# Performance work log

Hardware: AMD Instinct MI355X
Metric: run time of the kernel (lower is better)

## Reference

```python
import jax, jax.numpy as jnp
import numpy as np

N = 2_000_000
C = 64
B = 16
H = C // 2  # reduction_ratio = 2


def setup_inputs() -> dict:
    key = jax.random.key(0)
    k1, k2, k3, k4, k5, k6 = jax.random.split(key, 6)
    x = jax.random.normal(k1, (N, C), dtype=jnp.float32)
    batch_ids = jnp.sort(jax.random.randint(k2, (N,), 0, B, dtype=jnp.int32))
    # nn.Linear-style params: y = x @ W.T + b
    W1 = jax.random.normal(k3, (H, C), dtype=jnp.float32) * (1.0 / np.sqrt(C))
    b1 = jax.random.normal(k4, (H,), dtype=jnp.float32) * 0.01
    W2 = jax.random.normal(k5, (C, H), dtype=jnp.float32) * (1.0 / np.sqrt(H))
    b2 = jax.random.normal(k6, (C,), dtype=jnp.float32) * 0.01
    return {"x": x, "batch_ids": batch_ids, "W1": W1, "b1": b1, "W2": W2, "b2": b2}


def reference(x, batch_ids, W1, b1, W2, b2):
    # Global avg / max pooling per batch segment -> [B, C]
    sums = jax.ops.segment_sum(x, batch_ids, num_segments=B)
    counts = jax.ops.segment_sum(jnp.ones((x.shape[0],), x.dtype), batch_ids, num_segments=B)
    avg = sums / jnp.maximum(counts, 1.0)[:, None]
    mx = jax.ops.segment_max(x, batch_ids, num_segments=B)

    def mlp(h):  # shared tiny MLP: Linear -> ReLU -> Linear
        return jax.nn.relu(h @ W1.T + b1) @ W2.T + b2

    att = jax.nn.sigmoid(mlp(avg) + mlp(mx))  # [B, C]
    # per-point broadcast multiply-add: x * att[batch] + x
    return x * att[batch_ids] + x
```

## Files before the change

kernel.cpp:

```cpp
#include <hip/hip_runtime.h>
#include <math.h>

#define NCH   64
#define NBAT  16
#define NHID  32
#define NBLK  1024

typedef float    f4 __attribute__((ext_vector_type(4)));
typedef _Float16 h4 __attribute__((ext_vector_type(4)));


__device__ __forceinline__ void atomicMaxF(float* addr, float v) {
    if (v >= 0.0f) atomicMax((int*)addr, __float_as_int(v));
    else           atomicMin((unsigned int*)addr, __float_as_uint(v));
}

__device__ __forceinline__ f4 vmax4(f4 a, f4 b) {
    f4 r;
    r.x = fmaxf(a.x, b.x); r.y = fmaxf(a.y, b.y);
    r.z = fmaxf(a.z, b.z); r.w = fmaxf(a.w, b.w);
    return r;
}

__device__ __forceinline__ int lower_bound_i(const int* __restrict__ a, int n, int v) {
    int lo = 0, hi = n;
    while (lo < hi) {
        const int mid = (lo + hi) >> 1;
        if (a[mid] < v) lo = mid + 1; else hi = mid;
    }
    return lo;
}

__global__ __launch_bounds__(256) void init_kernel(float* ws) {
    const int i = blockIdx.x * blockDim.x + threadIdx.x;
    if (i < 1024) {
        ws[i] = 0.0f;
        ws[1024 + i] = -INFINITY;
    }
}


__global__ __launch_bounds__(256) void pool_stage_kernel(const float* __restrict__ x,
                                                         const int* __restrict__ bid,
                                                         float* __restrict__ wsum,
                                                         float* __restrict__ wmax,
                                                         _Float16* __restrict__ xh,
                                                         int n, int rpb) {
    __shared__ int sstart[NBAT + 1];
    __shared__ f4 ls[256];
    __shared__ f4 lm[256];
    const int t = threadIdx.x;
    if (t <= NBAT) sstart[t] = (t == NBAT) ? n : lower_bound_i(bid, n, t);
    __syncthreads();

    const int c4 = t & 15;
    const int rg = t >> 4;
    const int r0 = blockIdx.x * rpb;
    const int rend = min(r0 + rpb, n);
    const f4 fzero = {0.f, 0.f, 0.f, 0.f};
    const f4 fninf = {-INFINITY, -INFINITY, -INFINITY, -INFINITY};

    for (int b = 0; b < NBAT; ++b) {
        const int lo = max(sstart[b], r0);
        const int hi = min(sstart[b + 1], rend);
        if (lo >= hi) continue;

        f4 s = fzero, m = fninf;
        const int base = lo + rg;
        const int k = (hi > base) ? ((hi - base + 15) >> 4) : 0;
        const float* xp = x + (size_t)base * NCH + c4 * 4;
        _Float16* hp = xh + (size_t)base * NCH + c4 * 4;
        int j = 0;
        for (; j + 4 <= k; j += 4) {
            const f4 v0 = __builtin_nontemporal_load(reinterpret_cast<const f4*>(xp + (size_t)(j + 0) * 16 * NCH));
            const f4 v1 = __builtin_nontemporal_load(reinterpret_cast<const f4*>(xp + (size_t)(j + 1) * 16 * NCH));
            const f4 v2 = __builtin_nontemporal_load(reinterpret_cast<const f4*>(xp + (size_t)(j + 2) * 16 * NCH));
            const f4 v3 = __builtin_nontemporal_load(reinterpret_cast<const f4*>(xp + (size_t)(j + 3) * 16 * NCH));
            s += v0; s += v1; s += v2; s += v3;
            m = vmax4(m, vmax4(vmax4(v0, v1), vmax4(v2, v3)));
            *reinterpret_cast<h4*>(hp + (size_t)(j + 0) * 16 * NCH) = __builtin_convertvector(v0, h4);
            *reinterpret_cast<h4*>(hp + (size_t)(j + 1) * 16 * NCH) = __builtin_convertvector(v1, h4);
            *reinterpret_cast<h4*>(hp + (size_t)(j + 2) * 16 * NCH) = __builtin_convertvector(v2, h4);
            *reinterpret_cast<h4*>(hp + (size_t)(j + 3) * 16 * NCH) = __builtin_convertvector(v3, h4);
        }
        for (; j < k; ++j) {
            const f4 v = __builtin_nontemporal_load(reinterpret_cast<const f4*>(xp + (size_t)j * 16 * NCH));
            s += v; m = vmax4(m, v);
            *reinterpret_cast<h4*>(hp + (size_t)j * 16 * NCH) = __builtin_convertvector(v, h4);
        }

        ls[t] = s; lm[t] = m;
        __syncthreads();
        if (rg == 0) {
            for (int gg = 1; gg < 16; ++gg) {
                s += ls[gg * 16 + c4];
                m = vmax4(m, lm[gg * 16 + c4]);
            }
            float* ps = wsum + b * NCH + c4 * 4;
            atomicAdd(ps + 0, s.x);
            atomicAdd(ps + 1, s.y);
            atomicAdd(ps + 2, s.z);
            atomicAdd(ps + 3, s.w);
            float* pm = wmax + b * NCH + c4 * 4;
            atomicMaxF(pm + 0, m.x);
            atomicMaxF(pm + 1, m.y);
            atomicMaxF(pm + 2, m.z);
            atomicMaxF(pm + 3, m.w);
        }
        __syncthreads();
    }
}

__global__ __launch_bounds__(256) void apply_stage_kernel(const _Float16* __restrict__ xh,
                                                          const int* __restrict__ bid,
                                                          const float* __restrict__ scale,
                                                          float* __restrict__ out,
                                                          int n, int rpb) {
    __shared__ int   sstart[NBAT + 1];
    __shared__ float s_scale[NBAT * NCH];
    const int t = threadIdx.x;
    if (t <= NBAT) sstart[t] = (t == NBAT) ? n : lower_bound_i(bid, n, t);
    for (int i = t; i < NBAT * NCH; i += 256) s_scale[i] = scale[i];
    __syncthreads();

    const int c4 = t & 15;
    const int rg = t >> 4;
    const int r0 = blockIdx.x * rpb;
    const int rend = min(r0 + rpb, n);

    for (int b = 0; b < NBAT; ++b) {
        const int lo = max(sstart[b], r0);
        const int hi = min(sstart[b + 1], rend);
        if (lo >= hi) continue;

        const f4 sc = *reinterpret_cast<const f4*>(s_scale + b * NCH + c4 * 4);
        const int base = lo + rg;
        const int k = (hi > base) ? ((hi - base + 15) >> 4) : 0;
        const _Float16* hp = xh + (size_t)base * NCH + c4 * 4;
        float* op = out + (size_t)base * NCH + c4 * 4;

        int j = 0;
        for (; j + 8 <= k; j += 8) {
            h4 u[8];
#pragma unroll
            for (int q = 0; q < 8; ++q)
                u[q] = *reinterpret_cast<const h4*>(hp + (size_t)(j + q) * 16 * NCH);
#pragma unroll
            for (int q = 0; q < 8; ++q) {
                const f4 v = __builtin_convertvector(u[q], f4) * sc;
                __builtin_nontemporal_store(v, reinterpret_cast<f4*>(op + (size_t)(j + q) * 16 * NCH));
            }
        }
        for (; j < k; ++j) {
            const h4 u = *reinterpret_cast<const h4*>(hp + (size_t)j * 16 * NCH);
            const f4 v = __builtin_convertvector(u, f4) * sc;
            __builtin_nontemporal_store(v, reinterpret_cast<f4*>(op + (size_t)j * 16 * NCH));
        }
    }
}


__global__ __launch_bounds__(256) void pool_kernel(const float* __restrict__ x,
                                                   const int* __restrict__ bid,
                                                   float* __restrict__ wsum,
                                                   float* __restrict__ wmax,
                                                   int n, int rpb) {
    __shared__ int sstart[NBAT + 1];
    __shared__ f4 ls[256];
    __shared__ f4 lm[256];
    const int t = threadIdx.x;
    if (t <= NBAT) sstart[t] = (t == NBAT) ? n : lower_bound_i(bid, n, t);
    __syncthreads();

    const int c4 = t & 15;
    const int rg = t >> 4;
    const int r0 = blockIdx.x * rpb;
    const int rend = min(r0 + rpb, n);
    const f4 fzero = {0.f, 0.f, 0.f, 0.f};
    const f4 fninf = {-INFINITY, -INFINITY, -INFINITY, -INFINITY};

    for (int b = 0; b < NBAT; ++b) {
        const int lo = max(sstart[b], r0);
        const int hi = min(sstart[b + 1], rend);
        if (lo >= hi) continue;

        f4 s = fzero, m = fninf;
        const int base = lo + rg;
        const int k = (hi > base) ? ((hi - base + 15) >> 4) : 0;
        const float* xp = x + (size_t)base * NCH + c4 * 4;
        int j = 0;
        for (; j + 4 <= k; j += 4) {
            const f4 v0 = *reinterpret_cast<const f4*>(xp + (size_t)(j + 0) * 16 * NCH);
            const f4 v1 = *reinterpret_cast<const f4*>(xp + (size_t)(j + 1) * 16 * NCH);
            const f4 v2 = *reinterpret_cast<const f4*>(xp + (size_t)(j + 2) * 16 * NCH);
            const f4 v3 = *reinterpret_cast<const f4*>(xp + (size_t)(j + 3) * 16 * NCH);
            s += v0; s += v1; s += v2; s += v3;
            m = vmax4(m, vmax4(vmax4(v0, v1), vmax4(v2, v3)));
        }
        for (; j < k; ++j) {
            const f4 v = *reinterpret_cast<const f4*>(xp + (size_t)j * 16 * NCH);
            s += v; m = vmax4(m, v);
        }

        ls[t] = s; lm[t] = m;
        __syncthreads();
        if (rg == 0) {
            for (int gg = 1; gg < 16; ++gg) {
                s += ls[gg * 16 + c4];
                m = vmax4(m, lm[gg * 16 + c4]);
            }
            float* ps = wsum + b * NCH + c4 * 4;
            atomicAdd(ps + 0, s.x);
            atomicAdd(ps + 1, s.y);
            atomicAdd(ps + 2, s.z);
            atomicAdd(ps + 3, s.w);
            float* pm = wmax + b * NCH + c4 * 4;
            atomicMaxF(pm + 0, m.x);
            atomicMaxF(pm + 1, m.y);
            atomicMaxF(pm + 2, m.z);
            atomicMaxF(pm + 3, m.w);
        }
        __syncthreads();
    }
}

__global__ __launch_bounds__(256) void apply_kernel(const float* __restrict__ x,
                                                    const int* __restrict__ bid,
                                                    const float* __restrict__ scale,
                                                    float* __restrict__ out,
                                                    int n, int rpb) {
    __shared__ int   sstart[NBAT + 1];
    __shared__ float s_scale[NBAT * NCH];
    const int t = threadIdx.x;
    if (t <= NBAT) sstart[t] = (t == NBAT) ? n : lower_bound_i(bid, n, t);
    for (int i = t; i < NBAT * NCH; i += 256) s_scale[i] = scale[i];
    __syncthreads();

    const int c4 = t & 15;
    const int rg = t >> 4;
    const int r0 = blockIdx.x * rpb;
    const int rend = min(r0 + rpb, n);

    for (int b = NBAT - 1; b >= 0; --b) {
        const int lo = max(sstart[b], r0);
        const int hi = min(sstart[b + 1], rend);
        if (lo >= hi) continue;

        const f4 sc = *reinterpret_cast<const f4*>(s_scale + b * NCH + c4 * 4);
        const int base = lo + rg;
        int k = (hi > base) ? ((hi - base + 15) >> 4) : 0;
        const float* xp = x + (size_t)base * NCH + c4 * 4;
        float* op = out + (size_t)base * NCH + c4 * 4;

        while (k >= 4) {
            k -= 4;
            const f4 v0 = *reinterpret_cast<const f4*>(xp + (size_t)(k + 0) * 16 * NCH);
            const f4 v1 = *reinterpret_cast<const f4*>(xp + (size_t)(k + 1) * 16 * NCH);
            const f4 v2 = *reinterpret_cast<const f4*>(xp + (size_t)(k + 2) * 16 * NCH);
            const f4 v3 = *reinterpret_cast<const f4*>(xp + (size_t)(k + 3) * 16 * NCH);
            __builtin_nontemporal_store(v0 * sc, reinterpret_cast<f4*>(op + (size_t)(k + 0) * 16 * NCH));
            __builtin_nontemporal_store(v1 * sc, reinterpret_cast<f4*>(op + (size_t)(k + 1) * 16 * NCH));
            __builtin_nontemporal_store(v2 * sc, reinterpret_cast<f4*>(op + (size_t)(k + 2) * 16 * NCH));
            __builtin_nontemporal_store(v3 * sc, reinterpret_cast<f4*>(op + (size_t)(k + 3) * 16 * NCH));
        }
        while (k > 0) {
            --k;
            const f4 v = *reinterpret_cast<const f4*>(xp + (size_t)k * 16 * NCH);
            __builtin_nontemporal_store(v * sc, reinterpret_cast<f4*>(op + (size_t)k * 16 * NCH));
        }
    }
}


__global__ __launch_bounds__(512) void mlp_kernel(const float* __restrict__ ws,
                                                  const int* __restrict__ bid,
                                                  const float* __restrict__ W1,
                                                  const float* __restrict__ b1,
                                                  const float* __restrict__ W2,
                                                  const float* __restrict__ b2,
                                                  float* __restrict__ scale_out,
                                                  int n) {
    __shared__ int   sstart[NBAT + 1];
    __shared__ float avg[NBAT * NCH];
    __shared__ float mxs[NBAT * NCH];
    __shared__ float h1a[NBAT * NHID];
    __shared__ float h1m[NBAT * NHID];
    const int t = threadIdx.x;
    if (t <= NBAT) sstart[t] = (t == NBAT) ? n : lower_bound_i(bid, n, t);
    __syncthreads();

    for (int i = t; i < NBAT * NCH; i += 512) {
        const int b = i >> 6;
        const float c = (float)(sstart[b + 1] - sstart[b]);
        avg[i] = ws[i] / fmaxf(c, 1.0f);
        mxs[i] = ws[1024 + i];
    }
    __syncthreads();

    {
        const int b = t >> 5, j = t & 31;
        float sa = b1[j], sm = b1[j];
        const float* w = W1 + j * NCH;
        for (int c = 0; c < NCH; ++c) {
            const float wv = w[c];
            sa += avg[b * NCH + c] * wv;
            sm += mxs[b * NCH + c] * wv;
        }
        h1a[b * NHID + j] = fmaxf(sa, 0.0f);
        h1m[b * NHID + j] = fmaxf(sm, 0.0f);
    }
    __syncthreads();

    for (int i = t; i < NBAT * NCH; i += 512) {
        const int b = i >> 6, c = i & 63;
        float ya = b2[c], ym = b2[c];
        const float* w = W2 + c * NHID;
        for (int j = 0; j < NHID; ++j) {
            const float wv = w[j];
            ya += h1a[b * NHID + j] * wv;
            ym += h1m[b * NHID + j] * wv;
        }
        const float z = ya + ym;
        const float sig = 1.0f / (1.0f + expf(-z));
        scale_out[i] = 1.0f + sig;
    }
}

extern "C" void kernel_launch(void* const* d_in, const int* in_sizes, int n_in,
                              void* d_out, int out_size, void* d_ws, size_t ws_size,
                              hipStream_t stream) {
    const float* x   = (const float*)d_in[0];
    const int*   bid = (const int*)d_in[1];
    const float* W1  = (const float*)d_in[2];
    const float* b1  = (const float*)d_in[3];
    const float* W2  = (const float*)d_in[4];
    const float* b2  = (const float*)d_in[5];
    float* out = (float*)d_out;
    const int n = in_sizes[1];

    float* ws     = (float*)d_ws;
    float* wsum   = ws;
    float* wmax   = ws + 1024;
    float* wscale = ws + 2064;
    _Float16* xh  = (_Float16*)((char*)d_ws + 16384);

    const size_t need = 16384 + (size_t)n * NCH * sizeof(_Float16);
    const bool staged = (ws_size >= need);

    hipLaunchKernelGGL(init_kernel, dim3(4), dim3(256), 0, stream, ws);

    const int rpb = (n + NBLK - 1) / NBLK;
    if (staged) {
        hipLaunchKernelGGL(pool_stage_kernel, dim3(NBLK), dim3(256), 0, stream,
                           x, bid, wsum, wmax, xh, n, rpb);
        hipLaunchKernelGGL(mlp_kernel, dim3(1), dim3(512), 0, stream,
                           ws, bid, W1, b1, W2, b2, wscale, n);
        hipLaunchKernelGGL(apply_stage_kernel, dim3(NBLK), dim3(256), 0, stream,
                           xh, bid, wscale, out, n, rpb);
    } else {
        hipLaunchKernelGGL(pool_kernel, dim3(NBLK), dim3(256), 0, stream,
                           x, bid, wsum, wmax, n, rpb);
        hipLaunchKernelGGL(mlp_kernel, dim3(1), dim3(512), 0, stream,
                           ws, bid, W1, b1, W2, b2, wscale, n);
        hipLaunchKernelGGL(apply_kernel, dim3(NBLK), dim3(256), 0, stream,
                           x, bid, wscale, out, n, rpb);
    }
}
```

Measured before the change: 275.3 us.

## Fuse MLP into staged apply kernel and widen fp16 loads to 8 lanes

```diff
diff --git a/kernel.cpp b/kernel.cpp
--- a/kernel.cpp
+++ b/kernel.cpp
@@ -7,7 +7,9 @@
 #define NBLK  1024
 
 typedef float    f4 __attribute__((ext_vector_type(4)));
+typedef float    f8 __attribute__((ext_vector_type(8)));
 typedef _Float16 h4 __attribute__((ext_vector_type(4)));
+typedef _Float16 h8 __attribute__((ext_vector_type(8)));
 
 
 __device__ __forceinline__ void atomicMaxF(float* addr, float v) {
@@ -113,18 +115,59 @@
 
 __global__ __launch_bounds__(256) void apply_stage_kernel(const _Float16* __restrict__ xh,
                                                           const int* __restrict__ bid,
-                                                          const float* __restrict__ scale,
+                                                          const float* __restrict__ ws,
+                                                          const float* __restrict__ W1,
+                                                          const float* __restrict__ b1,
+                                                          const float* __restrict__ W2,
+                                                          const float* __restrict__ b2,
                                                           float* __restrict__ out,
                                                           int n, int rpb) {
     __shared__ int   sstart[NBAT + 1];
+    __shared__ float avg[NBAT * NCH];
+    __shared__ float mxs[NBAT * NCH];
+    __shared__ float h1a[NBAT * NHID];
+    __shared__ float h1m[NBAT * NHID];
     __shared__ float s_scale[NBAT * NCH];
     const int t = threadIdx.x;
     if (t <= NBAT) sstart[t] = (t == NBAT) ? n : lower_bound_i(bid, n, t);
-    for (int i = t; i < NBAT * NCH; i += 256) s_scale[i] = scale[i];
-    __syncthreads();
-
-    const int c4 = t & 15;
-    const int rg = t >> 4;
+    __syncthreads();
+
+    for (int i = t; i < NBAT * NCH; i += 256) {
+        const int b = i >> 6;
+        const float c = (float)(sstart[b + 1] - sstart[b]);
+        avg[i] = ws[i] / fmaxf(c, 1.0f);
+        mxs[i] = ws[1024 + i];
+    }
+    __syncthreads();
+    for (int j2 = t; j2 < NBAT * NHID; j2 += 256) {
+        const int b = j2 >> 5, j = j2 & 31;
+        float sa = b1[j], sm = b1[j];
+        const float* w = W1 + j * NCH;
+        for (int c = 0; c < NCH; ++c) {
+            const float wv = w[c];
+            sa += avg[b * NCH + c] * wv;
+            sm += mxs[b * NCH + c] * wv;
+        }
+        h1a[j2] = fmaxf(sa, 0.0f);
+        h1m[j2] = fmaxf(sm, 0.0f);
+    }
+    __syncthreads();
+    for (int i = t; i < NBAT * NCH; i += 256) {
+        const int b = i >> 6, c = i & 63;
+        float ya = b2[c], ym = b2[c];
+        const float* w = W2 + c * NHID;
+        for (int j = 0; j < NHID; ++j) {
+            const float wv = w[j];
+            ya += h1a[b * NHID + j] * wv;
+            ym += h1m[b * NHID + j] * wv;
+        }
+        const float z = ya + ym;
+        s_scale[i] = 1.0f + 1.0f / (1.0f + expf(-z));
+    }
+    __syncthreads();
+
+    const int c8 = t & 7;
+    const int rg = t >> 3;
     const int r0 = blockIdx.x * rpb;
     const int rend = min(r0 + rpb, n);
 
@@ -133,28 +176,31 @@
         const int hi = min(sstart[b + 1], rend);
         if (lo >= hi) continue;
 
-        const f4 sc = *reinterpret_cast<const f4*>(s_scale + b * NCH + c4 * 4);
+        const f8 sc = *reinterpret_cast<const f8*>(s_scale + b * NCH + c8 * 8);
         const int base = lo + rg;
-        const int k = (hi > base) ? ((hi - base + 15) >> 4) : 0;
-        const _Float16* hp = xh + (size_t)base * NCH + c4 * 4;
-        float* op = out + (size_t)base * NCH + c4 * 4;
+        const int k = (hi > base) ? ((hi - base + 31) >> 5) : 0;
+        const _Float16* hp = xh + (size_t)base * NCH + c8 * 8;
+        float* op = out + (size_t)base * NCH + c8 * 8;
 
         int j = 0;
-        for (; j + 8 <= k; j += 8) {
-            h4 u[8];
-#pragma unroll
-            for (int q = 0; q < 8; ++q)
-                u[q] = *reinterpret_cast<const h4*>(hp + (size_t)(j + q) * 16 * NCH);
-#pragma unroll
-            for (int q = 0; q < 8; ++q) {
-                const f4 v = __builtin_convertvector(u[q], f4) * sc;
-                __builtin_nontemporal_store(v, reinterpret_cast<f4*>(op + (size_t)(j + q) * 16 * NCH));
-            }
+        for (; j + 4 <= k; j += 4) {
+            h8 u0 = *reinterpret_cast<const h8*>(hp + (size_t)(j + 0) * 32 * NCH);
+            h8 u1 = *reinterpret_cast<const h8*>(hp + (size_t)(j + 1) * 32 * NCH);
+            h8 u2 = *reinterpret_cast<const h8*>(hp + (size_t)(j + 2) * 32 * NCH);
+            h8 u3 = *reinterpret_cast<const h8*>(hp + (size_t)(j + 3) * 32 * NCH);
+            __builtin_nontemporal_store(__builtin_convertvector(u0, f8) * sc,
+                                        reinterpret_cast<f8*>(op + (size_t)(j + 0) * 32 * NCH));
+            __builtin_nontemporal_store(__builtin_convertvector(u1, f8) * sc,
+                                        reinterpret_cast<f8*>(op + (size_t)(j + 1) * 32 * NCH));
+            __builtin_nontemporal_store(__builtin_convertvector(u2, f8) * sc,
+                                        reinterpret_cast<f8*>(op + (size_t)(j + 2) * 32 * NCH));
+            __builtin_nontemporal_store(__builtin_convertvector(u3, f8) * sc,
+                                        reinterpret_cast<f8*>(op + (size_t)(j + 3) * 32 * NCH));
         }
         for (; j < k; ++j) {
-            const h4 u = *reinterpret_cast<const h4*>(hp + (size_t)j * 16 * NCH);
-            const f4 v = __builtin_convertvector(u, f4) * sc;
-            __builtin_nontemporal_store(v, reinterpret_cast<f4*>(op + (size_t)j * 16 * NCH));
+            const h8 u = *reinterpret_cast<const h8*>(hp + (size_t)j * 32 * NCH);
+            __builtin_nontemporal_store(__builtin_convertvector(u, f8) * sc,
+                                        reinterpret_cast<f8*>(op + (size_t)j * 32 * NCH));
         }
     }
 }
@@ -224,54 +270,6 @@
     }
 }
 
-__global__ __launch_bounds__(256) void apply_kernel(const float* __restrict__ x,
-                                                    const int* __restrict__ bid,
-                                                    const float* __restrict__ scale,
-                                                    float* __restrict__ out,
-                                                    int n, int rpb) {
-    __shared__ int   sstart[NBAT + 1];
-    __shared__ float s_scale[NBAT * NCH];
-    const int t = threadIdx.x;
-    if (t <= NBAT) sstart[t] = (t == NBAT) ? n : lower_bound_i(bid, n, t);
-    for (int i = t; i < NBAT * NCH; i += 256) s_scale[i] = scale[i];
-    __syncthreads();
-
-    const int c4 = t & 15;
-    const int rg = t >> 4;
-    const int r0 = blockIdx.x * rpb;
-    const int rend = min(r0 + rpb, n);
-
-    for (int b = NBAT - 1; b >= 0; --b) {
-        const int lo = max(sstart[b], r0);
-        const int hi = min(sstart[b + 1], rend);
-        if (lo >= hi) continue;
-
-        const f4 sc = *reinterpret_cast<const f4*>(s_scale + b * NCH + c4 * 4);
-        const int base = lo + rg;
-        int k = (hi > base) ? ((hi - base + 15) >> 4) : 0;
-        const float* xp = x + (size_t)base * NCH + c4 * 4;
-        float* op = out + (size_t)base * NCH + c4 * 4;
-
-        while (k >= 4) {
-            k -= 4;
-            const f4 v0 = *reinterpret_cast<const f4*>(xp + (size_t)(k + 0) * 16 * NCH);
-            const f4 v1 = *reinterpret_cast<const f4*>(xp + (size_t)(k + 1) * 16 * NCH);
-            const f4 v2 = *reinterpret_cast<const f4*>(xp + (size_t)(k + 2) * 16 * NCH);
-            const f4 v3 = *reinterpret_cast<const f4*>(xp + (size_t)(k + 3) * 16 * NCH);
-            __builtin_nontemporal_store(v0 * sc, reinterpret_cast<f4*>(op + (size_t)(k + 0) * 16 * NCH));
-            __builtin_nontemporal_store(v1 * sc, reinterpret_cast<f4*>(op + (size_t)(k + 1) * 16 * NCH));
-            __builtin_nontemporal_store(v2 * sc, reinterpret_cast<f4*>(op + (size_t)(k + 2) * 16 * NCH));
-            __builtin_nontemporal_store(v3 * sc, reinterpret_cast<f4*>(op + (size_t)(k + 3) * 16 * NCH));
-        }
-        while (k > 0) {
-            --k;
-            const f4 v = *reinterpret_cast<const f4*>(xp + (size_t)k * 16 * NCH);
-            __builtin_nontemporal_store(v * sc, reinterpret_cast<f4*>(op + (size_t)k * 16 * NCH));
-        }
-    }
-}
-
-
 __global__ __launch_bounds__(512) void mlp_kernel(const float* __restrict__ ws,
                                                   const int* __restrict__ bid,
                                                   const float* __restrict__ W1,
@@ -326,6 +324,53 @@
     }
 }
 
+__global__ __launch_bounds__(256) void apply_kernel(const float* __restrict__ x,
+                                                    const int* __restrict__ bid,
+                                                    const float* __restrict__ scale,
+                                                    float* __restrict__ out,
+                                                    int n, int rpb) {
+    __shared__ int   sstart[NBAT + 1];
+    __shared__ float s_scale[NBAT * NCH];
+    const int t = threadIdx.x;
+    if (t <= NBAT) sstart[t] = (t == NBAT) ? n : lower_bound_i(bid, n, t);
+    for (int i = t; i < NBAT * NCH; i += 256) s_scale[i] = scale[i];
+    __syncthreads();
+
+    const int c4 = t & 15;
+    const int rg = t >> 4;
+    const int r0 = blockIdx.x * rpb;
+    const int rend = min(r0 + rpb, n);
+
+    for (int b = NBAT - 1; b >= 0; --b) {
+        const int lo = max(sstart[b], r0);
+        const int hi = min(sstart[b + 1], rend);
+        if (lo >= hi) continue;
+
+        const f4 sc = *reinterpret_cast<const f4*>(s_scale + b * NCH + c4 * 4);
+        const int base = lo + rg;
+        int k = (hi > base) ? ((hi - base + 15) >> 4) : 0;
+        const float* xp = x + (size_t)base * NCH + c4 * 4;
+        float* op = out + (size_t)base * NCH + c4 * 4;
+
+        while (k >= 4) {
+            k -= 4;
+            const f4 v0 = *reinterpret_cast<const f4*>(xp + (size_t)(k + 0) * 16 * NCH);
+            const f4 v1 = *reinterpret_cast<const f4*>(xp + (size_t)(k + 1) * 16 * NCH);
+            const f4 v2 = *reinterpret_cast<const f4*>(xp + (size_t)(k + 2) * 16 * NCH);
+            const f4 v3 = *reinterpret_cast<const f4*>(xp + (size_t)(k + 3) * 16 * NCH);
+            __builtin_nontemporal_store(v0 * sc, reinterpret_cast<f4*>(op + (size_t)(k + 0) * 16 * NCH));
+            __builtin_nontemporal_store(v1 * sc, reinterpret_cast<f4*>(op + (size_t)(k + 1) * 16 * NCH));
+            __builtin_nontemporal_store(v2 * sc, reinterpret_cast<f4*>(op + (size_t)(k + 2) * 16 * NCH));
+            __builtin_nontemporal_store(v3 * sc, reinterpret_cast<f4*>(op + (size_t)(k + 3) * 16 * NCH));
+        }
+        while (k > 0) {
+            --k;
+            const f4 v = *reinterpret_cast<const f4*>(xp + (size_t)k * 16 * NCH);
+            __builtin_nontemporal_store(v * sc, reinterpret_cast<f4*>(op + (size_t)k * 16 * NCH));
+        }
+    }
+}
+
 extern "C" void kernel_launch(void* const* d_in, const int* in_sizes, int n_in,
                               void* d_out, int out_size, void* d_ws, size_t ws_size,
                               hipStream_t stream) {
@@ -353,10 +398,8 @@
     if (staged) {
         hipLaunchKernelGGL(pool_stage_kernel, dim3(NBLK), dim3(256), 0, stream,
                            x, bid, wsum, wmax, xh, n, rpb);
-        hipLaunchKernelGGL(mlp_kernel, dim3(1), dim3(512), 0, stream,
-                           ws, bid, W1, b1, W2, b2, wscale, n);
         hipLaunchKernelGGL(apply_stage_kernel, dim3(NBLK), dim3(256), 0, stream,
-                           xh, bid, wscale, out, n, rpb);
+                           xh, bid, ws, W1, b1, W2, b2, out, n, rpb);
     } else {
         hipLaunchKernelGGL(pool_kernel, dim3(NBLK), dim3(256), 0, stream,
                            x, bid, wsum, wmax, n, rpb);
```

New measurement: 360.1 us. 30.8% more time.
